# Kernel tuning notes

Hardware: AMD Instinct MI355X
Metric: run time of the kernel (lower is better)

## Reference

```python
import jax, jax.numpy as jnp
import numpy as np

PS = 3          # patch_size
ALPHA = 0.5     # alpha_0 (no step() calls -> stays at init value)
A_CUBIC = -0.75 # torch bicubic kernel coefficient


def _cubic_w(t):
    at = jnp.abs(t)
    w1 = ((A_CUBIC + 2.0) * at - (A_CUBIC + 3.0)) * at * at + 1.0
    w2 = A_CUBIC * (((at - 5.0) * at + 8.0) * at - 4.0)
    return jnp.where(at <= 1.0, w1, jnp.where(at < 2.0, w2, 0.0))


def _resize_axis(x, out_size, axis):
    # bicubic, align_corners=True, border-clamped (matches torch.nn.functional.interpolate)
    in_size = x.shape[axis]
    scale = (in_size - 1) / (out_size - 1)
    coords = jnp.arange(out_size, dtype=x.dtype) * jnp.asarray(scale, x.dtype)
    i0 = jnp.floor(coords)
    frac = coords - i0
    offs = jnp.arange(-1, 3)
    idx = jnp.clip(i0.astype(jnp.int32)[:, None] + offs[None, :], 0, in_size - 1)
    w = _cubic_w(frac[:, None] - offs[None, :].astype(x.dtype))  # [out,4]
    xm = jnp.moveaxis(x, axis, -1)
    vals = xm[..., idx]                      # [..., out, 4]
    out = jnp.einsum('...ot,ot->...o', vals, w)
    return jnp.moveaxis(out, -1, axis)


def _bicubic(x, out_h, out_w):
    return _resize_axis(_resize_axis(x, out_h, 2), out_w, 3)


def _unfold(x, ps=PS):
    # [B,C,H,W] -> [B, (H/ps)*(W/ps), C, ps, ps], row-major over (H-chunk, W-chunk)
    B, C, H, W = x.shape
    x = x.reshape(B, C, H // ps, ps, W // ps, ps)
    x = x.transpose(0, 2, 4, 1, 3, 5)
    return x.reshape(B, -1, C, ps, ps)


def _fold(p, C, H, W, ps=PS):
    B = p.shape[0]
    x = p.reshape(B, H // ps, W // ps, C, ps, ps)
    x = x.transpose(0, 3, 1, 4, 2, 5)
    return x.reshape(B, C, H, W)


def _g_database(tar, ps=PS):
    B, C, H, W = tar.shape
    scales = [tar, _bicubic(tar, H // 2, W // 2), _bicubic(tar, H // 4, W // 4)]
    patches = []
    for i in range(1, ps):
        for j in range(1, ps):
            for s in scales:
                h, w = s.shape[2], s.shape[3]
                if ps < min(h, w):
                    patches.append(_unfold(s[:, :, i:h - (ps - i), j:w - (ps - j)], ps))
    for s in scales:
        patches.append(_unfold(s, ps))
    return jnp.concatenate(patches, axis=1)  # [B, G, C, ps, ps]


def setup_inputs() -> dict:
    key = jax.random.key(0)
    k1, k2 = jax.random.split(key)
    inp = jax.random.uniform(k1, (2, 3, 144, 144), dtype=jnp.float32)
    tar = jax.random.uniform(k2, (2, 3, 144, 144), dtype=jnp.float32)
    return {"inp": inp, "tar": tar}


def reference(inp, tar):
    B, C, H, W = tar.shape
    ps = PS
    D = C * ps * ps
    ipf = _unfold(inp, ps).reshape(B, -1, D)   # [B,N,D]
    tpf = _unfold(tar, ps).reshape(B, -1, D)
    gf = _g_database(tar, ps).reshape(B, -1, D)  # [B,G,D]

    # nearest-candidate selection is done under no_grad in the original
    gf_s = jax.lax.stop_gradient(gf)
    tpf_s = jax.lax.stop_gradient(tpf)
    ipf_s = jax.lax.stop_gradient(ipf)
    gn = jnp.sum(gf_s * gf_s, axis=-1)  # [B,G]

    def sqdist(a):  # sum of squared diffs over D: [B,G,N]
        an = jnp.sum(a * a, axis=-1)
        return an[:, None, :] + gn[:, :, None] - 2.0 * jnp.einsum('bnd,bgd->bgn', a, gf_s)

    l = ALPHA * sqdist(tpf_s) + (1.0 - ALPHA) * sqdist(ipf_s)  # [B,G,N]
    index = jnp.argmin(l, axis=1)                              # [B,N]
    sel = jnp.take_along_axis(gf_s, index[..., None], axis=1)  # [B,N,D]

    loss_p = jnp.abs(ipf - sel)  # L1Loss(reduction='none')
    loss_img = _fold(loss_p.reshape(B, -1, C, ps, ps), C, H, W, ps)
    sel_img = _fold(sel.reshape(B, -1, C, ps, ps), C, H, W, ps)
    return loss_img.mean(), sel_img
```

## Files before the change

### kernel.cpp

```cpp
#include <hip/hip_runtime.h>
#include <math.h>

#define A_CUBIC (-0.75f)
#define NB 2
#define NC 3
#define HH 144
#define NPB 2304
#define GG 14460
#define DD 27
#define DP 28
#define GSPLIT 128
#define GTILE 113

typedef float v2f __attribute__((ext_vector_type(2)));

__constant__ int c_seg_start[15] = {0,2209,2738,2859,5068,5597,5718,7927,8456,8577,10786,11315,11436,13740,14316};
__constant__ int c_seg_gw[15]    = {47,23,11, 47,23,11, 47,23,11, 47,23,11, 48,24,12};
__constant__ int c_seg_oy[15]    = {1,1,1, 1,1,1, 2,2,2, 2,2,2, 0,0,0};
__constant__ int c_seg_ox[15]    = {1,1,1, 2,2,2, 1,1,1, 2,2,2, 0,0,0};
__constant__ int c_seg_src[15]   = {0,1,2, 0,1,2, 0,1,2, 0,1,2, 0,1,2};

__device__ __forceinline__ float cubicw(float t) {
    float at = fabsf(t);
    if (at <= 1.0f) return ((A_CUBIC + 2.0f) * at - (A_CUBIC + 3.0f)) * at * at + 1.0f;
    if (at < 2.0f)  return A_CUBIC * (((at - 5.0f) * at + 8.0f) * at - 4.0f);
    return 0.0f;
}

__global__ void prep_k(const float* __restrict__ tar, const float* __restrict__ inp,
                       float* __restrict__ s1, float* __restrict__ s2,
                       float* __restrict__ m, unsigned long long* __restrict__ best) {
    int t = blockIdx.x * 256 + threadIdx.x;
    const int total1 = NB * NC * 72 * 72;
    const int total2 = NB * NC * 36 * 36;
    if (t < total1 + total2) {
        float* dst; int O; int idx;
        if (t < total1) { dst = s1; O = 72; idx = t; }
        else            { dst = s2; O = 36; idx = t - total1; }
        int x  = idx % O;
        int y  = (idx / O) % O;
        int bc = idx / (O * O);
        const float* src = tar + (size_t)bc * HH * HH;
        float scale = (float)(143.0 / (double)(O - 1));
        float fy = (float)y * scale;
        float iyf = floorf(fy); float fry = fy - iyf; int iy = (int)iyf;
        float fx = (float)x * scale;
        float ixf = floorf(fx); float frx = fx - ixf; int ix = (int)ixf;
        float wy[4], wx[4];
        #pragma unroll
        for (int d = 0; d < 4; ++d) {
            wy[d] = cubicw(fry - (float)(d - 1));
            wx[d] = cubicw(frx - (float)(d - 1));
        }
        float acc = 0.0f;
        #pragma unroll
        for (int dx = 0; dx < 4; ++dx) {
            int cx = min(max(ix - 1 + dx, 0), HH - 1);
            float inner = 0.0f;
            #pragma unroll
            for (int dy = 0; dy < 4; ++dy) {
                int cy = min(max(iy - 1 + dy, 0), HH - 1);
                inner += wy[dy] * src[cy * HH + cx];
            }
            acc += wx[dx] * inner;
        }
        dst[idx] = acc;
    } else {
        int u = t - (total1 + total2);
        if (u >= NB * NPB) return;
        int b = u / NPB, n = u % NPB;
        int hc = n / 48, wc = n % 48;
        const float* ib = inp + (size_t)b * NC * HH * HH;
        const float* tb = tar + (size_t)b * NC * HH * HH;
        float* row = m + (size_t)u * DP;
        #pragma unroll
        for (int c = 0; c < 3; ++c)
            #pragma unroll
            for (int dy = 0; dy < 3; ++dy)
                #pragma unroll
                for (int dx = 0; dx < 3; ++dx) {
                    int off = (c * HH + hc * 3 + dy) * HH + wc * 3 + dx;
                    row[(c * 3 + dy) * 3 + dx] = ib[off] + tb[off];
                }
        row[27] = -1.0f;
        best[u] = 0ULL;
    }
}

__global__ void build_gf_k(const float* __restrict__ tar, const float* __restrict__ s1,
                           const float* __restrict__ s2, float* __restrict__ gf) {
    int t = blockIdx.x * 256 + threadIdx.x;
    if (t >= NB * GG) return;
    int b = t / GG, g = t % GG;
    int s = 0;
    #pragma unroll
    for (int k = 1; k < 15; ++k) if (g >= c_seg_start[k]) s = k;
    int p  = g - c_seg_start[s];
    int gw = c_seg_gw[s];
    int hc = p / gw, wc = p % gw;
    int oy = c_seg_oy[s], ox = c_seg_ox[s];
    int srci = c_seg_src[s];
    const float* img; int sz;
    if (srci == 0)      { img = tar; sz = 144; }
    else if (srci == 1) { img = s1;  sz = 72;  }
    else                { img = s2;  sz = 36;  }
    const float* base = img + (size_t)b * NC * sz * sz;
    int y0 = oy + hc * 3, x0 = ox + wc * 3;
    float acc = 0.0f;
    float* row = gf + (size_t)t * DP;
    #pragma unroll
    for (int c = 0; c < 3; ++c)
        #pragma unroll
        for (int dy = 0; dy < 3; ++dy)
            #pragma unroll
            for (int dx = 0; dx < 3; ++dx) {
                float v = base[((size_t)c * sz + y0 + dy) * sz + x0 + dx];
                row[(c * 3 + dy) * 3 + dx] = v;
                acc = fmaf(v, v, acc);
            }
    row[27] = acc;
}

__device__ __forceinline__ void dot28x3(const v2f r0[14], const v2f r1[14], const v2f r2[14],
                                        const v2f gR[14], float& s0, float& s1, float& s2) {
    v2f a0 = {0.0f, 0.0f}, a1 = {0.0f, 0.0f}, a2 = {0.0f, 0.0f};
    #pragma unroll
    for (int i = 0; i < 14; ++i) {
        a0 = __builtin_elementwise_fma(r0[i], gR[i], a0);
        a1 = __builtin_elementwise_fma(r1[i], gR[i], a1);
        a2 = __builtin_elementwise_fma(r2[i], gR[i], a2);
    }
    s0 = a0.x + a0.y; s1 = a1.x + a1.y; s2 = a2.x + a2.y;
}

__global__ __launch_bounds__(256, 4) void argmin_k(
        const float* __restrict__ gf, const float* __restrict__ m,
        unsigned long long* __restrict__ best) {
    int tid = threadIdx.x;
    int nb = blockIdx.y;
    int b  = nb / 3;
    int n0 = nb * 768 + tid;
    const v2f* m0 = (const v2f*)(m + (size_t)n0 * DP);
    const v2f* m1 = (const v2f*)(m + (size_t)(n0 + 256) * DP);
    const v2f* m2 = (const v2f*)(m + (size_t)(n0 + 512) * DP);
    v2f r0[14], r1[14], r2[14];
    #pragma unroll
    for (int i = 0; i < 14; ++i) { r0[i] = m0[i]; r1[i] = m1[i]; r2[i] = m2[i]; }
    int g0 = blockIdx.x * GTILE;
    int g1 = min(g0 + GTILE, GG);
    const float* gfb = gf + (size_t)b * GG * DP;
    float bv0 = -3.0e38f, bv1 = -3.0e38f, bv2 = -3.0e38f;
    int   bi0 = 0,        bi1 = 0,        bi2 = 0;

    v2f A[14], B[14];
    {
        const v2f* p = (const v2f*)(gfb + (size_t)g0 * DP);
        #pragma unroll
        for (int i = 0; i < 14; ++i) A[i] = p[i];
    }
    int g = g0;
    for (; g + 1 < g1; g += 2) {
        {
            const v2f* p = (const v2f*)(gfb + (size_t)(g + 1) * DP);
            #pragma unroll
            for (int i = 0; i < 14; ++i) B[i] = p[i];
        }
        float s0, s1, s2;
        dot28x3(r0, r1, r2, A, s0, s1, s2);
        if (s0 > bv0) { bv0 = s0; bi0 = g; }
        if (s1 > bv1) { bv1 = s1; bi1 = g; }
        if (s2 > bv2) { bv2 = s2; bi2 = g; }
        {
            const v2f* p = (const v2f*)(gfb + (size_t)(g + 2) * DP);
            #pragma unroll
            for (int i = 0; i < 14; ++i) A[i] = p[i];
        }
        dot28x3(r0, r1, r2, B, s0, s1, s2);
        if (s0 > bv0) { bv0 = s0; bi0 = g + 1; }
        if (s1 > bv1) { bv1 = s1; bi1 = g + 1; }
        if (s2 > bv2) { bv2 = s2; bi2 = g + 1; }
    }
    if (g < g1) {
        float s0, s1, s2;
        dot28x3(r0, r1, r2, A, s0, s1, s2);
        if (s0 > bv0) { bv0 = s0; bi0 = g; }
        if (s1 > bv1) { bv1 = s1; bi1 = g; }
        if (s2 > bv2) { bv2 = s2; bi2 = g; }
    }
    unsigned u0 = __float_as_uint(bv0); u0 ^= (unsigned)(((int)u0 >> 31)) | 0x80000000u;
    unsigned u1 = __float_as_uint(bv1); u1 ^= (unsigned)(((int)u1 >> 31)) | 0x80000000u;
    unsigned u2 = __float_as_uint(bv2); u2 ^= (unsigned)(((int)u2 >> 31)) | 0x80000000u;
    atomicMax(&best[n0],       ((unsigned long long)u0 << 32) | (unsigned)(~bi0));
    atomicMax(&best[n0 + 256], ((unsigned long long)u1 << 32) | (unsigned)(~bi1));
    atomicMax(&best[n0 + 512], ((unsigned long long)u2 << 32) | (unsigned)(~bi2));
}

__global__ void finalize_k(const float* __restrict__ gf,
                           const unsigned long long* __restrict__ best,
                           const float* __restrict__ inp,
                           float* __restrict__ out, float* __restrict__ lpart) {
    __shared__ float red[256];
    int t = blockIdx.x * 256 + threadIdx.x;
    float lsum = 0.0f;
    if (t < NB * NPB) {
        int b = t / NPB, n = t % NPB;
        unsigned long long pk = best[t];
        int bi = (int)(~(unsigned)(pk & 0xFFFFFFFFull));
        int hc = n / 48, wc = n % 48;
        const float* grow = gf + ((size_t)b * GG + bi) * DP;
        const float* ib   = inp + (size_t)b * NC * HH * HH;
        float* sel = out + 1 + (size_t)b * NC * HH * HH;
        #pragma unroll
        for (int c = 0; c < 3; ++c)
            #pragma unroll
            for (int dy = 0; dy < 3; ++dy)
                #pragma unroll
                for (int dx = 0; dx < 3; ++dx) {
                    int d = (c * 3 + dy) * 3 + dx;
                    float sv = grow[d];
                    int off = (c * HH + hc * 3 + dy) * HH + wc * 3 + dx;
                    sel[off] = sv;
                    lsum += fabsf(ib[off] - sv);
                }
    }
    red[threadIdx.x] = lsum;
    __syncthreads();
    for (int s = 128; s > 0; s >>= 1) {
        if (threadIdx.x < s) red[threadIdx.x] += red[threadIdx.x + s];
        __syncthreads();
    }
    if (threadIdx.x == 0) lpart[blockIdx.x] = red[0];
}

__global__ void sum_k(const float* __restrict__ lpart, float* __restrict__ out) {
    if (threadIdx.x == 0) {
        float s = 0.0f;
        for (int i = 0; i < 18; ++i) s += lpart[i];
        out[0] = s * (1.0f / 124416.0f);
    }
}

extern "C" void kernel_launch(void* const* d_in, const int* in_sizes, int n_in,
                              void* d_out, int out_size, void* d_ws, size_t ws_size,
                              hipStream_t stream) {
    const float* inp = (const float*)d_in[0];
    const float* tar = (const float*)d_in[1];
    float* out = (float*)d_out;
    float* ws  = (float*)d_ws;

    float* s1 = ws;
    float* s2 = s1 + 31104;
    float* gf = s2 + 7776;
    float* m  = gf + 809760;
    unsigned long long* best = (unsigned long long*)(m + 129024);
    float* lp = (float*)(best + 4608);

    prep_k    <<<(43488 + 255) / 256, 256, 0, stream>>>(tar, inp, s1, s2, m, best);
    build_gf_k<<<(28920 + 255) / 256, 256, 0, stream>>>(tar, s1, s2, gf);
    argmin_k  <<<dim3(GSPLIT, 6), 256, 0, stream>>>(gf, m, best);
    finalize_k<<<18, 256, 0, stream>>>(gf, best, inp, out, lp);
    sum_k     <<<1, 64, 0, stream>>>(lp, out);
}
```

Baseline: 66.49 us.

## Stage database tile in LDS and double the G-split for argmin

The argmin kernel now copies its slice of gallery patches into shared memory once per block and reads them from LDS, instead of each thread streaming them through global/scalar loads with manual double-buffering. The G dimension is split into twice as many tiles (GSPLIT 256, GTILE 57) to raise the number of blocks. The dot product switches from packed v2f FMAs to scalar float4-based FMAs with four partial accumulators. In exchange it adds a __syncthreads, more atomics per output, and may lose the packed-FMA throughput.

```diff
diff --git a/kernel.cpp b/kernel.cpp
--- a/kernel.cpp
+++ b/kernel.cpp
@@ -9,10 +9,8 @@
 #define GG 14460
 #define DD 27
 #define DP 28
-#define GSPLIT 128
-#define GTILE 113
-
-typedef float v2f __attribute__((ext_vector_type(2)));
+#define GSPLIT 256
+#define GTILE 57
 
 __constant__ int c_seg_start[15] = {0,2209,2738,2859,5068,5597,5718,7927,8456,8577,10786,11315,11436,13740,14316};
 __constant__ int c_seg_gw[15]    = {47,23,11, 47,23,11, 47,23,11, 47,23,11, 48,24,12};
@@ -121,78 +119,71 @@
     row[27] = acc;
 }
 
-__device__ __forceinline__ void dot28x3(const v2f r0[14], const v2f r1[14], const v2f r2[14],
-                                        const v2f gR[14], float& s0, float& s1, float& s2) {
-    v2f a0 = {0.0f, 0.0f}, a1 = {0.0f, 0.0f}, a2 = {0.0f, 0.0f};
-    #pragma unroll
-    for (int i = 0; i < 14; ++i) {
-        a0 = __builtin_elementwise_fma(r0[i], gR[i], a0);
-        a1 = __builtin_elementwise_fma(r1[i], gR[i], a1);
-        a2 = __builtin_elementwise_fma(r2[i], gR[i], a2);
-    }
-    s0 = a0.x + a0.y; s1 = a1.x + a1.y; s2 = a2.x + a2.y;
-}
-
-__global__ __launch_bounds__(256, 4) void argmin_k(
-        const float* __restrict__ gf, const float* __restrict__ m,
-        unsigned long long* __restrict__ best) {
+__global__ __launch_bounds__(256) __attribute__((amdgpu_waves_per_eu(1, 4)))
+void argmin_k(const float* __restrict__ gf, const float* __restrict__ m,
+              unsigned long long* __restrict__ best) {
+    __shared__ __align__(16) float glds[GTILE * DP];
     int tid = threadIdx.x;
     int nb = blockIdx.y;
     int b  = nb / 3;
     int n0 = nb * 768 + tid;
-    const v2f* m0 = (const v2f*)(m + (size_t)n0 * DP);
-    const v2f* m1 = (const v2f*)(m + (size_t)(n0 + 256) * DP);
-    const v2f* m2 = (const v2f*)(m + (size_t)(n0 + 512) * DP);
-    v2f r0[14], r1[14], r2[14];
-    #pragma unroll
-    for (int i = 0; i < 14; ++i) { r0[i] = m0[i]; r1[i] = m1[i]; r2[i] = m2[i]; }
+
+    float4 mr0[7], mr1[7], mr2[7];
+    {
+        const float4* p0 = (const float4*)(m + (size_t)n0 * DP);
+        const float4* p1 = (const float4*)(m + (size_t)(n0 + 256) * DP);
+        const float4* p2 = (const float4*)(m + (size_t)(n0 + 512) * DP);
+        #pragma unroll
+        for (int i = 0; i < 7; ++i) { mr0[i] = p0[i]; mr1[i] = p1[i]; mr2[i] = p2[i]; }
+    }
+
     int g0 = blockIdx.x * GTILE;
     int g1 = min(g0 + GTILE, GG);
-    const float* gfb = gf + (size_t)b * GG * DP;
+    int nload = g1 - g0; if (nload < 0) nload = 0;
+
+    {
+        const float4* src = (const float4*)(gf + ((size_t)b * GG + g0) * DP);
+        float4* dst = (float4*)glds;
+        for (int k = tid; k < nload * 7; k += 256) dst[k] = src[k];
+    }
+    __syncthreads();
+
     float bv0 = -3.0e38f, bv1 = -3.0e38f, bv2 = -3.0e38f;
     int   bi0 = 0,        bi1 = 0,        bi2 = 0;
 
-    v2f A[14], B[14];
-    {
-        const v2f* p = (const v2f*)(gfb + (size_t)g0 * DP);
-        #pragma unroll
-        for (int i = 0; i < 14; ++i) A[i] = p[i];
-    }
-    int g = g0;
-    for (; g + 1 < g1; g += 2) {
-        {
-            const v2f* p = (const v2f*)(gfb + (size_t)(g + 1) * DP);
-            #pragma unroll
-            for (int i = 0; i < 14; ++i) B[i] = p[i];
+    for (int j = 0; j < nload; ++j) {
+        const float4* gr = (const float4*)&glds[j * DP];
+        float a00, a01, a02, a03, a10, a11, a12, a13, a20, a21, a22, a23;
+        float4 gv = gr[0];
+        a00 = mr0[0].x * gv.x; a01 = mr0[0].y * gv.y; a02 = mr0[0].z * gv.z; a03 = mr0[0].w * gv.w;
+        a10 = mr1[0].x * gv.x; a11 = mr1[0].y * gv.y; a12 = mr1[0].z * gv.z; a13 = mr1[0].w * gv.w;
+        a20 = mr2[0].x * gv.x; a21 = mr2[0].y * gv.y; a22 = mr2[0].z * gv.z; a23 = mr2[0].w * gv.w;
+        #pragma unroll
+        for (int i = 1; i < 7; ++i) {
+            gv = gr[i];
+            a00 = fmaf(mr0[i].x, gv.x, a00); a01 = fmaf(mr0[i].y, gv.y, a01);
+            a02 = fmaf(mr0[i].z, gv.z, a02); a03 = fmaf(mr0[i].w, gv.w, a03);
+            a10 = fmaf(mr1[i].x, gv.x, a10); a11 = fmaf(mr1[i].y, gv.y, a11);
+            a12 = fmaf(mr1[i].z, gv.z, a12); a13 = fmaf(mr1[i].w, gv.w, a13);
+            a20 = fmaf(mr2[i].x, gv.x, a20); a21 = fmaf(mr2[i].y, gv.y, a21);
+            a22 = fmaf(mr2[i].z, gv.z, a22); a23 = fmaf(mr2[i].w, gv.w, a23);
         }
-        float s0, s1, s2;
-        dot28x3(r0, r1, r2, A, s0, s1, s2);
-        if (s0 > bv0) { bv0 = s0; bi0 = g; }
-        if (s1 > bv1) { bv1 = s1; bi1 = g; }
-        if (s2 > bv2) { bv2 = s2; bi2 = g; }
-        {
-            const v2f* p = (const v2f*)(gfb + (size_t)(g + 2) * DP);
-            #pragma unroll
-            for (int i = 0; i < 14; ++i) A[i] = p[i];
-        }
-        dot28x3(r0, r1, r2, B, s0, s1, s2);
-        if (s0 > bv0) { bv0 = s0; bi0 = g + 1; }
-        if (s1 > bv1) { bv1 = s1; bi1 = g + 1; }
-        if (s2 > bv2) { bv2 = s2; bi2 = g + 1; }
-    }
-    if (g < g1) {
-        float s0, s1, s2;
-        dot28x3(r0, r1, r2, A, s0, s1, s2);
-        if (s0 > bv0) { bv0 = s0; bi0 = g; }
-        if (s1 > bv1) { bv1 = s1; bi1 = g; }
-        if (s2 > bv2) { bv2 = s2; bi2 = g; }
-    }
-    unsigned u0 = __float_as_uint(bv0); u0 ^= (unsigned)(((int)u0 >> 31)) | 0x80000000u;
-    unsigned u1 = __float_as_uint(bv1); u1 ^= (unsigned)(((int)u1 >> 31)) | 0x80000000u;
-    unsigned u2 = __float_as_uint(bv2); u2 ^= (unsigned)(((int)u2 >> 31)) | 0x80000000u;
-    atomicMax(&best[n0],       ((unsigned long long)u0 << 32) | (unsigned)(~bi0));
-    atomicMax(&best[n0 + 256], ((unsigned long long)u1 << 32) | (unsigned)(~bi1));
-    atomicMax(&best[n0 + 512], ((unsigned long long)u2 << 32) | (unsigned)(~bi2));
+        float s0 = (a00 + a01) + (a02 + a03);
+        float s1 = (a10 + a11) + (a12 + a13);
+        float s2 = (a20 + a21) + (a22 + a23);
+        int gg = g0 + j;
+        if (s0 > bv0) { bv0 = s0; bi0 = gg; }
+        if (s1 > bv1) { bv1 = s1; bi1 = gg; }
+        if (s2 > bv2) { bv2 = s2; bi2 = gg; }
+    }
+    if (nload > 0) {
+        unsigned u0 = __float_as_uint(bv0); u0 ^= (unsigned)(((int)u0 >> 31)) | 0x80000000u;
+        unsigned u1 = __float_as_uint(bv1); u1 ^= (unsigned)(((int)u1 >> 31)) | 0x80000000u;
+        unsigned u2 = __float_as_uint(bv2); u2 ^= (unsigned)(((int)u2 >> 31)) | 0x80000000u;
+        atomicMax(&best[n0],       ((unsigned long long)u0 << 32) | (unsigned)(~bi0));
+        atomicMax(&best[n0 + 256], ((unsigned long long)u1 << 32) | (unsigned)(~bi1));
+        atomicMax(&best[n0 + 512], ((unsigned long long)u2 << 32) | (unsigned)(~bi2));
+    }
 }
 
 __global__ void finalize_k(const float* __restrict__ gf,
```

New measurement: 74.47 us. 12.0% more time.
